# Kernel tuning notes

Measured on AMD Instinct MI355X. Metric: run time of the kernel, lower is better.

The kernel has to match this reference:

```python
import jax, jax.numpy as jnp
import numpy as np

B, S, T = 512, 1024, 64

def setup_inputs() -> dict:
    key = jax.random.key(0)
    k1, k2, k3 = jax.random.split(key, 3)
    emissions = jax.random.normal(k1, (B, S, T), dtype=jnp.float32)
    tags = jax.random.randint(k2, (B, S), 0, T, dtype=jnp.int32)
    mask = jnp.ones((B, S), dtype=jnp.float32)
    transitions = jax.random.normal(k3, (T, T), dtype=jnp.float32)
    return {"emissions": emissions, "tags": tags, "mask": mask, "transitions": transitions}

def _gold_score(emissions, tags, mask, transitions):
    # emit score of the gold tag at each position: (B, S)
    e = jnp.take_along_axis(emissions, tags[:, :, None], axis=2)[:, :, 0]
    # NOTE: original indexes transitions[curr, prev]
    trans = transitions[tags[:, 1:], tags[:, :-1]]  # (B, S-1)
    score = e[:, 0] * mask[:, 0]
    score = score + jnp.sum((trans + e[:, 1:]) * mask[:, 1:], axis=1)
    return score

def _partition(emissions, mask, transitions):
    # init: emissions at t=0, masked (matches original, which multiplies score by mask[:,0])
    score0 = emissions[:, 0] * mask[:, 0][:, None]  # (B, T)
    emis_rest = jnp.swapaxes(emissions[:, 1:], 0, 1)  # (S-1, B, T)
    mask_rest = jnp.swapaxes(mask[:, 1:], 0, 1)       # (S-1, B)

    def step(score, xs):
        emit, m = xs  # (B, T), (B,)
        # next[b, j] = logsumexp_i(score[b, i] + transitions[i, j])
        nxt = jax.nn.logsumexp(score[:, :, None] + transitions[None, :, :], axis=1)
        score = nxt + emit * m[:, None]
        return score, None

    score, _ = jax.lax.scan(step, score0, (emis_rest, mask_rest))
    return jax.nn.logsumexp(score, axis=1)  # (B,)

def reference(emissions, tags, mask, transitions):
    gold = _gold_score(emissions, tags, mask, transitions)
    fwd = _partition(emissions, mask, transitions)
    return jnp.mean(fwd - gold)
```

## Files before the change

kernel.cpp:

```cpp
#include <hip/hip_runtime.h>

#define BB 512
#define SS 1024
#define TT 64

__device__ __forceinline__ float wsum64(float v) {
#pragma unroll
  for (int off = 32; off > 0; off >>= 1) v += __shfl_xor(v, off, 64);
  return v;
}

#define E_LIST(M) \
  M(0) M(1) M(2) M(3) M(4) M(5) M(6) M(7) \
  M(8) M(9) M(10) M(11) M(12) M(13) M(14) M(15) \
  M(16) M(17) M(18) M(19) M(20) M(21) M(22) M(23) \
  M(24) M(25) M(26) M(27) M(28) M(29) M(30) M(31) \
  M(32) M(33) M(34) M(35) M(36) M(37) M(38) M(39) \
  M(40) M(41) M(42) M(43) M(44) M(45) M(46) M(47) \
  M(48) M(49) M(50) M(51) M(52) M(53) M(54) M(55) \
  M(56) M(57) M(58) M(59) M(60) M(61) M(62) M(63)

#define RL(i) __int_as_float(__builtin_amdgcn_readlane(pb_, (i)))

#define FMA4(i0, i1, i2, i3)          \
  a0 = fmaf(RL(i0), E##i0, a0);       \
  a1 = fmaf(RL(i1), E##i1, a1);       \
  a2 = fmaf(RL(i2), E##i2, a2);       \
  a3 = fmaf(RL(i3), E##i3, a3);

#define FMA_ALL                      \
  FMA4(0, 1, 2, 3)                   \
  FMA4(4, 5, 6, 7)                   \
  FMA4(8, 9, 10, 11)                 \
  FMA4(12, 13, 14, 15)               \
  FMA4(16, 17, 18, 19)               \
  FMA4(20, 21, 22, 23)               \
  FMA4(24, 25, 26, 27)               \
  FMA4(28, 29, 30, 31)               \
  FMA4(32, 33, 34, 35)               \
  FMA4(36, 37, 38, 39)               \
  FMA4(40, 41, 42, 43)               \
  FMA4(44, 45, 46, 47)               \
  FMA4(48, 49, 50, 51)               \
  FMA4(52, 53, 54, 55)               \
  FMA4(56, 57, 58, 59)               \
  FMA4(60, 61, 62, 63)

#define CRF_STEP(ev, mkv)                                                           \
  do {                                                                              \
    float f_ = __expf((ev) * (mkv));                                                \
    float pv_ = (DIR == 1) ? p * (f_ * inv) : p;                                    \
    int pb_ = __float_as_int(pv_);                                                  \
    float a0 = 0.f, a1 = 0.f, a2 = 0.f, a3 = 0.f;                                   \
    FMA_ALL                                                                         \
    float s_ = (a0 + a1) + (a2 + a3);                                               \
    p = (DIR == 0) ? s_ * (f_ * inv) : s_;                                          \
    float rn_ = __int_as_float(__builtin_amdgcn_readfirstlane(__float_as_int(s_))); \
    inv = __builtin_amdgcn_rcpf(rn_);                                               \
    float lg_ = __logf(rn_);                                                        \
    Lacc += lg_;                                                                    \
    lastlg = lg_;                                                                   \
  } while (0)

template <int DIR>
__device__ __forceinline__ void part_run(int b, int lane, const float* __restrict__ em,
                                         const float* __restrict__ mask,
                                         const float* __restrict__ trans,
                                         float* __restrict__ outv) {
  const float* tp = trans + (DIR == 0 ? lane : lane * TT);
#define EINIT(i) float E##i = __expf((DIR == 0) ? tp[(i)*TT] : tp[(i)]);
  E_LIST(EINIT)
#undef EINIT

  const float* emb = em + (size_t)b * SS * TT;
  const float* mkb = mask + (size_t)b * SS;

  constexpr int NST = (DIR == 0) ? (SS / 2 - 1) : (SS / 2);
  constexpr int S0 = (DIR == 0) ? 1 : (SS - 1);
  constexpr int SD = (DIR == 0) ? 1 : -1;
  constexpr int NG8 = NST / 8;
  constexpr int TAIL8 = NST & 7;

  float p = (DIR == 0) ? __expf(emb[lane] * mkb[0]) : 1.0f;
  float inv = 1.0f, Lacc = 0.0f, lastlg = 0.0f;

  float ebuf[8];
#pragma unroll
  for (int k = 0; k < 8; ++k) ebuf[k] = emb[(S0 + SD * k) * TT + lane];
  const float* ep = emb + (ptrdiff_t)(S0 + SD * 8) * TT + lane;

  float mv = 0.f;
  for (int t8 = 0; t8 < NG8; ++t8) {
    if ((t8 & 7) == 0) mv = mkb[S0 + SD * (t8 * 8 + lane)];
    int base = (t8 & 7) * 8;
#pragma unroll
    for (int k = 0; k < 8; ++k) {
      float e = ebuf[k];
      ebuf[k] = *ep;
      ep += SD * TT;
      float mk = __int_as_float(
          __builtin_amdgcn_readlane(__float_as_int(mv), base + k));
      CRF_STEP(e, mk);
    }
  }
  if constexpr (TAIL8 > 0) {
#pragma unroll
    for (int k = 0; k < TAIL8; ++k) {
      float e = ebuf[k];
      float mk = __int_as_float(
          __builtin_amdgcn_readlane(__float_as_int(mv), (NG8 & 7) * 8 + k));
      CRF_STEP(e, mk);
    }
  }

  outv[b * TT + lane] = __logf(p) + (Lacc - lastlg);
}

__global__ void __launch_bounds__(64, 1)
    fused_kernel(const float* __restrict__ em, const int* __restrict__ tags,
                 const float* __restrict__ mask, const float* __restrict__ trans,
                 float* __restrict__ alpha, float* __restrict__ beta,
                 float* __restrict__ gpart) {
  const int lane = threadIdx.x;
  const int bid = blockIdx.x;
  if (bid < 2 * BB) {
    const int b = bid >> 1;
    if ((bid & 1) == 0)
      part_run<0>(b, lane, em, mask, trans, alpha);
    else
      part_run<1>(b, lane, em, mask, trans, beta);
  } else {
    const int gid = bid - 2 * BB;
    const int b = gid >> 2, q = gid & 3;
    const int* tg = tags + b * SS;
    const float* mkb = mask + (size_t)b * SS;
    const float* emb = em + (size_t)b * SS * TT;
    float part = 0.f;
#pragma unroll
    for (int i = 0; i < 4; ++i) {
      int s = q * 256 + i * 64 + lane;
      int t1 = tg[s];
      float e = emb[s * TT + t1];
      float contrib = (s == 0) ? e : (trans[t1 * TT + tg[s - 1]] + e);
      part = fmaf(contrib, mkb[s], part);
    }
    part = wsum64(part);
    if (lane == 0) gpart[gid] = part;
  }
}

__global__ void combine_kernel(const float* __restrict__ alpha, const float* __restrict__ beta,
                               const float* __restrict__ gpart, float* __restrict__ out) {
  const int b = threadIdx.x;
  const float* av = alpha + b * TT;
  const float* bv = beta + b * TT;
  float m = -3.4e38f, s = 0.f;
#pragma unroll 8
  for (int j = 0; j < TT; ++j) {
    float v = av[j] + bv[j];
    float nm = fmaxf(m, v);
    s = s * __expf(m - nm) + __expf(v - nm);
    m = nm;
  }
  float Z = m + __logf(s);
  float g = gpart[4 * b] + gpart[4 * b + 1] + gpart[4 * b + 2] + gpart[4 * b + 3];
  float val = Z - g;
  val = wsum64(val);
  __shared__ float red[8];
  if ((threadIdx.x & 63) == 0) red[threadIdx.x >> 6] = val;
  __syncthreads();
  if (threadIdx.x == 0) {
    float t = 0.f;
#pragma unroll
    for (int w = 0; w < 8; ++w) t += red[w];
    out[0] = t * (1.0f / (float)BB);
  }
}

extern "C" void kernel_launch(void* const* d_in, const int* in_sizes, int n_in,
                              void* d_out, int out_size, void* d_ws, size_t ws_size,
                              hipStream_t stream) {
  const float* em = (const float*)d_in[0];
  const int* tags = (const int*)d_in[1];
  const float* mask = (const float*)d_in[2];
  const float* trans = (const float*)d_in[3];
  float* out = (float*)d_out;

  float* alpha = (float*)d_ws;
  float* beta = alpha + BB * TT;
  float* gpart = beta + BB * TT;

  fused_kernel<<<2 * BB + 4 * BB, TT, 0, stream>>>(em, tags, mask, trans, alpha, beta, gpart);
  combine_kernel<<<1, BB, 0, stream>>>(alpha, beta, gpart, out);
}
```

Before: 328.8 us.

## Broadcast recurrence state through LDS float4 reads instead of per-lane readlane

Each recurrence step now writes the 64-entry state vector to shared memory and reads it back as 16 broadcast float4 loads. This replaces 64 v_readlane scalar broadcasts per step, aiming to cut the scalar-broadcast cost and its associated hazards. The backward direction is restructured to apply the next position's emission factor before storing, which needs a one-step lookahead on emissions and mask. In exchange, an LDS write-then-read round trip now sits on the serial dependency chain of every step.

```diff
diff --git a/kernel.cpp b/kernel.cpp
--- a/kernel.cpp
+++ b/kernel.cpp
@@ -20,41 +20,48 @@
   M(48) M(49) M(50) M(51) M(52) M(53) M(54) M(55) \
   M(56) M(57) M(58) M(59) M(60) M(61) M(62) M(63)
 
-#define RL(i) __int_as_float(__builtin_amdgcn_readlane(pb_, (i)))
-
-#define FMA4(i0, i1, i2, i3)          \
-  a0 = fmaf(RL(i0), E##i0, a0);       \
-  a1 = fmaf(RL(i1), E##i1, a1);       \
-  a2 = fmaf(RL(i2), E##i2, a2);       \
-  a3 = fmaf(RL(i3), E##i3, a3);
-
-#define FMA_ALL                      \
-  FMA4(0, 1, 2, 3)                   \
-  FMA4(4, 5, 6, 7)                   \
-  FMA4(8, 9, 10, 11)                 \
-  FMA4(12, 13, 14, 15)               \
-  FMA4(16, 17, 18, 19)               \
-  FMA4(20, 21, 22, 23)               \
-  FMA4(24, 25, 26, 27)               \
-  FMA4(28, 29, 30, 31)               \
-  FMA4(32, 33, 34, 35)               \
-  FMA4(36, 37, 38, 39)               \
-  FMA4(40, 41, 42, 43)               \
-  FMA4(44, 45, 46, 47)               \
-  FMA4(48, 49, 50, 51)               \
-  FMA4(52, 53, 54, 55)               \
-  FMA4(56, 57, 58, 59)               \
-  FMA4(60, 61, 62, 63)
-
-#define CRF_STEP(ev, mkv)                                                           \
+#define RLF(v, i) __int_as_float(__builtin_amdgcn_readlane(__float_as_int(v), (i)))
+
+#define LOAD_ALLQ                                                     \
+  float4 q0 = pshv[0], q1 = pshv[1], q2 = pshv[2], q3 = pshv[3];      \
+  float4 q4 = pshv[4], q5 = pshv[5], q6 = pshv[6], q7 = pshv[7];      \
+  float4 q8 = pshv[8], q9 = pshv[9], q10 = pshv[10], q11 = pshv[11];  \
+  float4 q12 = pshv[12], q13 = pshv[13], q14 = pshv[14], q15 = pshv[15];
+
+#define FMAQ(qq, eA, eB, eC, eD) \
+  a0 = fmaf((qq).x, eA, a0);     \
+  a1 = fmaf((qq).y, eB, a1);     \
+  a2 = fmaf((qq).z, eC, a2);     \
+  a3 = fmaf((qq).w, eD, a3);
+
+#define FMA_ALLQ                     \
+  FMAQ(q0, E0, E1, E2, E3)           \
+  FMAQ(q1, E4, E5, E6, E7)           \
+  FMAQ(q2, E8, E9, E10, E11)         \
+  FMAQ(q3, E12, E13, E14, E15)       \
+  FMAQ(q4, E16, E17, E18, E19)       \
+  FMAQ(q5, E20, E21, E22, E23)       \
+  FMAQ(q6, E24, E25, E26, E27)       \
+  FMAQ(q7, E28, E29, E30, E31)       \
+  FMAQ(q8, E32, E33, E34, E35)       \
+  FMAQ(q9, E36, E37, E38, E39)       \
+  FMAQ(q10, E40, E41, E42, E43)      \
+  FMAQ(q11, E44, E45, E46, E47)      \
+  FMAQ(q12, E48, E49, E50, E51)      \
+  FMAQ(q13, E52, E53, E54, E55)      \
+  FMAQ(q14, E56, E57, E58, E59)      \
+  FMAQ(q15, E60, E61, E62, E63)
+
+#define CRF_STEP_FWD(ev, mkv)                                                       \
   do {                                                                              \
+    LOAD_ALLQ                                                                       \
     float f_ = __expf((ev) * (mkv));                                                \
-    float pv_ = (DIR == 1) ? p * (f_ * inv) : p;                                    \
-    int pb_ = __float_as_int(pv_);                                                  \
+    float fi_ = f_ * inv;                                                           \
     float a0 = 0.f, a1 = 0.f, a2 = 0.f, a3 = 0.f;                                   \
-    FMA_ALL                                                                         \
+    FMA_ALLQ                                                                        \
     float s_ = (a0 + a1) + (a2 + a3);                                               \
-    p = (DIR == 0) ? s_ * (f_ * inv) : s_;                                          \
+    p = s_ * fi_;                                                                   \
+    psh[lane] = p;                                                                  \
     float rn_ = __int_as_float(__builtin_amdgcn_readfirstlane(__float_as_int(s_))); \
     inv = __builtin_amdgcn_rcpf(rn_);                                               \
     float lg_ = __logf(rn_);                                                        \
@@ -62,11 +69,30 @@
     lastlg = lg_;                                                                   \
   } while (0)
 
+#define CRF_STEP_BWD(env, mknv)                                                     \
+  do {                                                                              \
+    LOAD_ALLQ                                                                       \
+    float fn_ = __expf((env) * (mknv));                                             \
+    float a0 = 0.f, a1 = 0.f, a2 = 0.f, a3 = 0.f;                                   \
+    FMA_ALLQ                                                                        \
+    float s_ = (a0 + a1) + (a2 + a3);                                               \
+    p = s_ * inv;                                                                   \
+    psh[lane] = p * fn_;                                                            \
+    float rn_ = __int_as_float(__builtin_amdgcn_readfirstlane(__float_as_int(s_))); \
+    inv = __builtin_amdgcn_rcpf(rn_);                                               \
+    float lg_ = __logf(rn_);                                                        \
+    Lacc += lg_;                                                                    \
+    lastlg = lg_;                                                                   \
+  } while (0)
+
 template <int DIR>
 __device__ __forceinline__ void part_run(int b, int lane, const float* __restrict__ em,
                                          const float* __restrict__ mask,
                                          const float* __restrict__ trans,
                                          float* __restrict__ outv) {
+  __shared__ float4 pshv[TT / 4];
+  float* psh = (float*)pshv;
+
   const float* tp = trans + (DIR == 0 ? lane : lane * TT);
 #define EINIT(i) float E##i = __expf((DIR == 0) ? tp[(i)*TT] : tp[(i)]);
   E_LIST(EINIT)
@@ -81,35 +107,55 @@
   constexpr int NG8 = NST / 8;
   constexpr int TAIL8 = NST & 7;
 
-  float p = (DIR == 0) ? __expf(emb[lane] * mkb[0]) : 1.0f;
-  float inv = 1.0f, Lacc = 0.0f, lastlg = 0.0f;
+  float p, inv = 1.0f, Lacc = 0.0f, lastlg = 0.0f;
 
   float ebuf[8];
 #pragma unroll
   for (int k = 0; k < 8; ++k) ebuf[k] = emb[(S0 + SD * k) * TT + lane];
   const float* ep = emb + (ptrdiff_t)(S0 + SD * 8) * TT + lane;
 
-  float mv = 0.f;
+  float mv = mkb[S0 + SD * lane];
+
+  if (DIR == 0) {
+    p = __expf(emb[lane] * mkb[0]);
+    psh[lane] = p;
+  } else {
+    p = 1.0f;
+    float mk1 = RLF(mv, 0);
+    float f1 = __expf(ebuf[0] * mk1);
+    psh[lane] = f1;
+  }
+
   for (int t8 = 0; t8 < NG8; ++t8) {
-    if ((t8 & 7) == 0) mv = mkb[S0 + SD * (t8 * 8 + lane)];
-    int base = (t8 & 7) * 8;
+    if (DIR == 0 && (t8 & 7) == 0) mv = mkb[S0 + SD * (t8 * 8 + lane)];
+    const int base = (t8 & 7) * 8;
 #pragma unroll
     for (int k = 0; k < 8; ++k) {
       float e = ebuf[k];
       ebuf[k] = *ep;
       ep += SD * TT;
-      float mk = __int_as_float(
-          __builtin_amdgcn_readlane(__float_as_int(mv), base + k));
-      CRF_STEP(e, mk);
+      if (DIR == 0) {
+        float mk = RLF(mv, base + k);
+        CRF_STEP_FWD(e, mk);
+      } else {
+        float mk_next;
+        if (base + k == 63) {
+          mv = mkb[S0 + SD * (t8 * 8 + 8 + lane)];
+          mk_next = RLF(mv, 0);
+        } else {
+          mk_next = RLF(mv, base + k + 1);
+        }
+        float e_next = ebuf[(k + 1) & 7];
+        CRF_STEP_BWD(e_next, mk_next);
+      }
     }
   }
   if constexpr (TAIL8 > 0) {
 #pragma unroll
     for (int k = 0; k < TAIL8; ++k) {
       float e = ebuf[k];
-      float mk = __int_as_float(
-          __builtin_amdgcn_readlane(__float_as_int(mv), (NG8 & 7) * 8 + k));
-      CRF_STEP(e, mk);
+      float mk = RLF(mv, (NG8 & 7) * 8 + k);
+      CRF_STEP_FWD(e, mk);
     }
   }
 
```

After: 376.5 us. 1.15x slower.

## Split each CRF recurrence step across two wavefronts with LDS exchange

Applied to the files above, without the earlier changes.

Each forward/backward chain now uses a 128-thread block where each wavefront holds half of the exp(transition) column (32 registers) and computes half of the 64-term dot product per step. The partial sums are exchanged through double-buffered shared memory with a __syncthreads every step. This halves the serial FMA/readlane chain per wave and lowers register pressure, but adds a block barrier and an LDS round trip on the critical path of every one of roughly 512 sequential steps. The gold-score blocks are adapted to 128 threads with a shared-memory reduction.

```diff
diff --git a/kernel.cpp b/kernel.cpp
--- a/kernel.cpp
+++ b/kernel.cpp
@@ -10,50 +10,41 @@
   return v;
 }
 
-#define E_LIST(M) \
+#define H_LIST(M) \
   M(0) M(1) M(2) M(3) M(4) M(5) M(6) M(7) \
   M(8) M(9) M(10) M(11) M(12) M(13) M(14) M(15) \
   M(16) M(17) M(18) M(19) M(20) M(21) M(22) M(23) \
-  M(24) M(25) M(26) M(27) M(28) M(29) M(30) M(31) \
-  M(32) M(33) M(34) M(35) M(36) M(37) M(38) M(39) \
-  M(40) M(41) M(42) M(43) M(44) M(45) M(46) M(47) \
-  M(48) M(49) M(50) M(51) M(52) M(53) M(54) M(55) \
-  M(56) M(57) M(58) M(59) M(60) M(61) M(62) M(63)
-
-#define RL(i) __int_as_float(__builtin_amdgcn_readlane(pb_, (i)))
-
-#define FMA4(i0, i1, i2, i3)          \
-  a0 = fmaf(RL(i0), E##i0, a0);       \
-  a1 = fmaf(RL(i1), E##i1, a1);       \
-  a2 = fmaf(RL(i2), E##i2, a2);       \
-  a3 = fmaf(RL(i3), E##i3, a3);
-
-#define FMA_ALL                      \
-  FMA4(0, 1, 2, 3)                   \
-  FMA4(4, 5, 6, 7)                   \
-  FMA4(8, 9, 10, 11)                 \
-  FMA4(12, 13, 14, 15)               \
-  FMA4(16, 17, 18, 19)               \
-  FMA4(20, 21, 22, 23)               \
-  FMA4(24, 25, 26, 27)               \
-  FMA4(28, 29, 30, 31)               \
-  FMA4(32, 33, 34, 35)               \
-  FMA4(36, 37, 38, 39)               \
-  FMA4(40, 41, 42, 43)               \
-  FMA4(44, 45, 46, 47)               \
-  FMA4(48, 49, 50, 51)               \
-  FMA4(52, 53, 54, 55)               \
-  FMA4(56, 57, 58, 59)               \
-  FMA4(60, 61, 62, 63)
-
-#define CRF_STEP(ev, mkv)                                                           \
+  M(24) M(25) M(26) M(27) M(28) M(29) M(30) M(31)
+
+#define RLW(i) __int_as_float(__builtin_amdgcn_readlane(pb_, (W) * 32 + (i)))
+
+#define FMAH4(i0, i1, i2, i3)    \
+  a0 = fmaf(RLW(i0), E##i0, a0); \
+  a1 = fmaf(RLW(i1), E##i1, a1); \
+  a2 = fmaf(RLW(i2), E##i2, a2); \
+  a3 = fmaf(RLW(i3), E##i3, a3);
+
+#define FMA_HALF        \
+  FMAH4(0, 1, 2, 3)     \
+  FMAH4(4, 5, 6, 7)     \
+  FMAH4(8, 9, 10, 11)   \
+  FMAH4(12, 13, 14, 15) \
+  FMAH4(16, 17, 18, 19) \
+  FMAH4(20, 21, 22, 23) \
+  FMAH4(24, 25, 26, 27) \
+  FMAH4(28, 29, 30, 31)
+
+#define CRF_STEP2(ev, mkv, BUF)                                                     \
   do {                                                                              \
     float f_ = __expf((ev) * (mkv));                                                \
     float pv_ = (DIR == 1) ? p * (f_ * inv) : p;                                    \
     int pb_ = __float_as_int(pv_);                                                  \
     float a0 = 0.f, a1 = 0.f, a2 = 0.f, a3 = 0.f;                                   \
-    FMA_ALL                                                                         \
-    float s_ = (a0 + a1) + (a2 + a3);                                               \
+    FMA_HALF                                                                        \
+    float h_ = (a0 + a1) + (a2 + a3);                                               \
+    xch[BUF][W][lane] = h_;                                                         \
+    __syncthreads();                                                                \
+    float s_ = h_ + xch[BUF][1 - W][lane];                                          \
     p = (DIR == 0) ? s_ * (f_ * inv) : s_;                                          \
     float rn_ = __int_as_float(__builtin_amdgcn_readfirstlane(__float_as_int(s_))); \
     inv = __builtin_amdgcn_rcpf(rn_);                                               \
@@ -62,14 +53,15 @@
     lastlg = lg_;                                                                   \
   } while (0)
 
-template <int DIR>
-__device__ __forceinline__ void part_run(int b, int lane, const float* __restrict__ em,
-                                         const float* __restrict__ mask,
-                                         const float* __restrict__ trans,
-                                         float* __restrict__ outv) {
+template <int DIR, int W>
+__device__ __forceinline__ void part_run2(int b, int lane, const float* __restrict__ em,
+                                          const float* __restrict__ mask,
+                                          const float* __restrict__ trans,
+                                          float* __restrict__ outv,
+                                          float (*xch)[2][TT]) {
   const float* tp = trans + (DIR == 0 ? lane : lane * TT);
-#define EINIT(i) float E##i = __expf((DIR == 0) ? tp[(i)*TT] : tp[(i)]);
-  E_LIST(EINIT)
+#define EINIT(i) float E##i = __expf((DIR == 0) ? tp[((W)*32 + (i)) * TT] : tp[(W)*32 + (i)]);
+  H_LIST(EINIT)
 #undef EINIT
 
   const float* emb = em + (size_t)b * SS * TT;
@@ -92,7 +84,7 @@
   float mv = 0.f;
   for (int t8 = 0; t8 < NG8; ++t8) {
     if ((t8 & 7) == 0) mv = mkb[S0 + SD * (t8 * 8 + lane)];
-    int base = (t8 & 7) * 8;
+    const int base = (t8 & 7) * 8;
 #pragma unroll
     for (int k = 0; k < 8; ++k) {
       float e = ebuf[k];
@@ -100,7 +92,11 @@
       ep += SD * TT;
       float mk = __int_as_float(
           __builtin_amdgcn_readlane(__float_as_int(mv), base + k));
-      CRF_STEP(e, mk);
+      if (k & 1) {
+        CRF_STEP2(e, mk, 1);
+      } else {
+        CRF_STEP2(e, mk, 0);
+      }
     }
   }
   if constexpr (TAIL8 > 0) {
@@ -109,26 +105,41 @@
       float e = ebuf[k];
       float mk = __int_as_float(
           __builtin_amdgcn_readlane(__float_as_int(mv), (NG8 & 7) * 8 + k));
-      CRF_STEP(e, mk);
-    }
-  }
-
-  outv[b * TT + lane] = __logf(p) + (Lacc - lastlg);
-}
-
-__global__ void __launch_bounds__(64, 1)
+      if (k & 1) {
+        CRF_STEP2(e, mk, 1);
+      } else {
+        CRF_STEP2(e, mk, 0);
+      }
+    }
+  }
+
+  if (W == 0) outv[b * TT + lane] = __logf(p) + (Lacc - lastlg);
+}
+
+__global__ void __launch_bounds__(128, 2)
     fused_kernel(const float* __restrict__ em, const int* __restrict__ tags,
                  const float* __restrict__ mask, const float* __restrict__ trans,
                  float* __restrict__ alpha, float* __restrict__ beta,
                  float* __restrict__ gpart) {
-  const int lane = threadIdx.x;
+  __shared__ float xch[2][2][TT];
+  __shared__ float gred[2];
+  const int tid = threadIdx.x;
   const int bid = blockIdx.x;
   if (bid < 2 * BB) {
     const int b = bid >> 1;
-    if ((bid & 1) == 0)
-      part_run<0>(b, lane, em, mask, trans, alpha);
-    else
-      part_run<1>(b, lane, em, mask, trans, beta);
+    const int lane = tid & 63;
+    const int w = tid >> 6;
+    if ((bid & 1) == 0) {
+      if (w == 0)
+        part_run2<0, 0>(b, lane, em, mask, trans, alpha, xch);
+      else
+        part_run2<0, 1>(b, lane, em, mask, trans, alpha, xch);
+    } else {
+      if (w == 0)
+        part_run2<1, 0>(b, lane, em, mask, trans, beta, xch);
+      else
+        part_run2<1, 1>(b, lane, em, mask, trans, beta, xch);
+    }
   } else {
     const int gid = bid - 2 * BB;
     const int b = gid >> 2, q = gid & 3;
@@ -137,15 +148,17 @@
     const float* emb = em + (size_t)b * SS * TT;
     float part = 0.f;
 #pragma unroll
-    for (int i = 0; i < 4; ++i) {
-      int s = q * 256 + i * 64 + lane;
+    for (int i = 0; i < 2; ++i) {
+      int s = q * 256 + i * 128 + tid;
       int t1 = tg[s];
       float e = emb[s * TT + t1];
       float contrib = (s == 0) ? e : (trans[t1 * TT + tg[s - 1]] + e);
       part = fmaf(contrib, mkb[s], part);
     }
     part = wsum64(part);
-    if (lane == 0) gpart[gid] = part;
+    if ((tid & 63) == 0) gred[tid >> 6] = part;
+    __syncthreads();
+    if (tid == 0) gpart[gid] = gred[0] + gred[1];
   }
 }
 
@@ -190,6 +203,6 @@
   float* beta = alpha + BB * TT;
   float* gpart = beta + BB * TT;
 
-  fused_kernel<<<2 * BB + 4 * BB, TT, 0, stream>>>(em, tags, mask, trans, alpha, beta, gpart);
+  fused_kernel<<<2 * BB + 4 * BB, 128, 0, stream>>>(em, tags, mask, trans, alpha, beta, gpart);
   combine_kernel<<<1, BB, 0, stream>>>(alpha, beta, gpart, out);
 }
```

Result: slower. 386.7 us (+17.6%).

## Process two batch sequences per wavefront to interleave independent recurrence chains

Applied to the files above, without the earlier changes.

Each partition wavefront now runs the forward or backward recurrence for two batch rows at once, interleaving their readlane and FMA chains. This halves the number of partition blocks from 1024 to 512 and gives the scheduler two independent dependency chains to hide readlane/FMA latency. The risk is reduced parallelism across CUs (512 waves on a 256-CU device) and higher register pressure from double state.

```diff
diff --git a/kernel.cpp b/kernel.cpp
--- a/kernel.cpp
+++ b/kernel.cpp
@@ -20,60 +20,102 @@
   M(48) M(49) M(50) M(51) M(52) M(53) M(54) M(55) \
   M(56) M(57) M(58) M(59) M(60) M(61) M(62) M(63)
 
-#define RL(i) __int_as_float(__builtin_amdgcn_readlane(pb_, (i)))
-
-#define FMA4(i0, i1, i2, i3)          \
-  a0 = fmaf(RL(i0), E##i0, a0);       \
-  a1 = fmaf(RL(i1), E##i1, a1);       \
-  a2 = fmaf(RL(i2), E##i2, a2);       \
-  a3 = fmaf(RL(i3), E##i3, a3);
-
-#define FMA_ALL                      \
-  FMA4(0, 1, 2, 3)                   \
-  FMA4(4, 5, 6, 7)                   \
-  FMA4(8, 9, 10, 11)                 \
-  FMA4(12, 13, 14, 15)               \
-  FMA4(16, 17, 18, 19)               \
-  FMA4(20, 21, 22, 23)               \
-  FMA4(24, 25, 26, 27)               \
-  FMA4(28, 29, 30, 31)               \
-  FMA4(32, 33, 34, 35)               \
-  FMA4(36, 37, 38, 39)               \
-  FMA4(40, 41, 42, 43)               \
-  FMA4(44, 45, 46, 47)               \
-  FMA4(48, 49, 50, 51)               \
-  FMA4(52, 53, 54, 55)               \
-  FMA4(56, 57, 58, 59)               \
-  FMA4(60, 61, 62, 63)
-
-#define CRF_STEP(ev, mkv)                                                           \
-  do {                                                                              \
-    float f_ = __expf((ev) * (mkv));                                                \
-    float pv_ = (DIR == 1) ? p * (f_ * inv) : p;                                    \
-    int pb_ = __float_as_int(pv_);                                                  \
-    float a0 = 0.f, a1 = 0.f, a2 = 0.f, a3 = 0.f;                                   \
-    FMA_ALL                                                                         \
-    float s_ = (a0 + a1) + (a2 + a3);                                               \
-    p = (DIR == 0) ? s_ * (f_ * inv) : s_;                                          \
-    float rn_ = __int_as_float(__builtin_amdgcn_readfirstlane(__float_as_int(s_))); \
-    inv = __builtin_amdgcn_rcpf(rn_);                                               \
-    float lg_ = __logf(rn_);                                                        \
-    Lacc += lg_;                                                                    \
-    lastlg = lg_;                                                                   \
+#define RLI(pb, i) __int_as_float(__builtin_amdgcn_readlane((pb), (i)))
+#define RLF(v, i) __int_as_float(__builtin_amdgcn_readlane(__float_as_int(v), (i)))
+
+#define GRP16(I0, I1, I2, I3, I4, I5, I6, I7, I8, I9, I10, I11, I12, I13, I14, I15) \
+  {                                                                                 \
+    float rA0 = RLI(pbA, I0), rA1 = RLI(pbA, I1), rA2 = RLI(pbA, I2),               \
+          rA3 = RLI(pbA, I3), rA4 = RLI(pbA, I4), rA5 = RLI(pbA, I5),               \
+          rA6 = RLI(pbA, I6), rA7 = RLI(pbA, I7), rA8 = RLI(pbA, I8),               \
+          rA9 = RLI(pbA, I9), rA10 = RLI(pbA, I10), rA11 = RLI(pbA, I11),           \
+          rA12 = RLI(pbA, I12), rA13 = RLI(pbA, I13), rA14 = RLI(pbA, I14),         \
+          rA15 = RLI(pbA, I15);                                                     \
+    float rB0 = RLI(pbB, I0), rB1 = RLI(pbB, I1), rB2 = RLI(pbB, I2),               \
+          rB3 = RLI(pbB, I3), rB4 = RLI(pbB, I4), rB5 = RLI(pbB, I5),               \
+          rB6 = RLI(pbB, I6), rB7 = RLI(pbB, I7), rB8 = RLI(pbB, I8),               \
+          rB9 = RLI(pbB, I9), rB10 = RLI(pbB, I10), rB11 = RLI(pbB, I11),           \
+          rB12 = RLI(pbB, I12), rB13 = RLI(pbB, I13), rB14 = RLI(pbB, I14),         \
+          rB15 = RLI(pbB, I15);                                                     \
+    aA0 = fmaf(rA0, E##I0, aA0);                                                    \
+    aA1 = fmaf(rA1, E##I1, aA1);                                                    \
+    aA2 = fmaf(rA2, E##I2, aA2);                                                    \
+    aA3 = fmaf(rA3, E##I3, aA3);                                                    \
+    aA0 = fmaf(rA4, E##I4, aA0);                                                    \
+    aA1 = fmaf(rA5, E##I5, aA1);                                                    \
+    aA2 = fmaf(rA6, E##I6, aA2);                                                    \
+    aA3 = fmaf(rA7, E##I7, aA3);                                                    \
+    aA0 = fmaf(rA8, E##I8, aA0);                                                    \
+    aA1 = fmaf(rA9, E##I9, aA1);                                                    \
+    aA2 = fmaf(rA10, E##I10, aA2);                                                  \
+    aA3 = fmaf(rA11, E##I11, aA3);                                                  \
+    aA0 = fmaf(rA12, E##I12, aA0);                                                  \
+    aA1 = fmaf(rA13, E##I13, aA1);                                                  \
+    aA2 = fmaf(rA14, E##I14, aA2);                                                  \
+    aA3 = fmaf(rA15, E##I15, aA3);                                                  \
+    aB0 = fmaf(rB0, E##I0, aB0);                                                    \
+    aB1 = fmaf(rB1, E##I1, aB1);                                                    \
+    aB2 = fmaf(rB2, E##I2, aB2);                                                    \
+    aB3 = fmaf(rB3, E##I3, aB3);                                                    \
+    aB0 = fmaf(rB4, E##I4, aB0);                                                    \
+    aB1 = fmaf(rB5, E##I5, aB1);                                                    \
+    aB2 = fmaf(rB6, E##I6, aB2);                                                    \
+    aB3 = fmaf(rB7, E##I7, aB3);                                                    \
+    aB0 = fmaf(rB8, E##I8, aB0);                                                    \
+    aB1 = fmaf(rB9, E##I9, aB1);                                                    \
+    aB2 = fmaf(rB10, E##I10, aB2);                                                  \
+    aB3 = fmaf(rB11, E##I11, aB3);                                                  \
+    aB0 = fmaf(rB12, E##I12, aB0);                                                  \
+    aB1 = fmaf(rB13, E##I13, aB1);                                                  \
+    aB2 = fmaf(rB14, E##I14, aB2);                                                  \
+    aB3 = fmaf(rB15, E##I15, aB3);                                                  \
+  }
+
+#define STEP_PAIR(eA, mkA, eB, mkB)                                                     \
+  do {                                                                                  \
+    float fA_ = __expf((eA) * (mkA));                                                   \
+    float fB_ = __expf((eB) * (mkB));                                                   \
+    float pvA_ = (DIR == 1) ? pA * (fA_ * invA) : pA;                                   \
+    float pvB_ = (DIR == 1) ? pB * (fB_ * invB) : pB;                                   \
+    int pbA = __float_as_int(pvA_);                                                     \
+    int pbB = __float_as_int(pvB_);                                                     \
+    float aA0 = 0.f, aA1 = 0.f, aA2 = 0.f, aA3 = 0.f;                                   \
+    float aB0 = 0.f, aB1 = 0.f, aB2 = 0.f, aB3 = 0.f;                                   \
+    GRP16(0, 1, 2, 3, 4, 5, 6, 7, 8, 9, 10, 11, 12, 13, 14, 15)                         \
+    GRP16(16, 17, 18, 19, 20, 21, 22, 23, 24, 25, 26, 27, 28, 29, 30, 31)               \
+    GRP16(32, 33, 34, 35, 36, 37, 38, 39, 40, 41, 42, 43, 44, 45, 46, 47)               \
+    GRP16(48, 49, 50, 51, 52, 53, 54, 55, 56, 57, 58, 59, 60, 61, 62, 63)               \
+    float sA_ = (aA0 + aA1) + (aA2 + aA3);                                              \
+    float sB_ = (aB0 + aB1) + (aB2 + aB3);                                              \
+    pA = (DIR == 0) ? sA_ * (fA_ * invA) : sA_;                                         \
+    pB = (DIR == 0) ? sB_ * (fB_ * invB) : sB_;                                         \
+    float rnA_ = __int_as_float(__builtin_amdgcn_readfirstlane(__float_as_int(sA_)));   \
+    float rnB_ = __int_as_float(__builtin_amdgcn_readfirstlane(__float_as_int(sB_)));   \
+    invA = __builtin_amdgcn_rcpf(rnA_);                                                 \
+    invB = __builtin_amdgcn_rcpf(rnB_);                                                 \
+    float lgA_ = __logf(rnA_);                                                          \
+    float lgB_ = __logf(rnB_);                                                          \
+    LaccA += lgA_;                                                                      \
+    LaccB += lgB_;                                                                      \
+    lastlgA = lgA_;                                                                     \
+    lastlgB = lgB_;                                                                     \
   } while (0)
 
 template <int DIR>
-__device__ __forceinline__ void part_run(int b, int lane, const float* __restrict__ em,
-                                         const float* __restrict__ mask,
-                                         const float* __restrict__ trans,
-                                         float* __restrict__ outv) {
+__device__ __forceinline__ void part_pair(int b0, int b1, int lane,
+                                          const float* __restrict__ em,
+                                          const float* __restrict__ mask,
+                                          const float* __restrict__ trans,
+                                          float* __restrict__ outv) {
   const float* tp = trans + (DIR == 0 ? lane : lane * TT);
 #define EINIT(i) float E##i = __expf((DIR == 0) ? tp[(i)*TT] : tp[(i)]);
   E_LIST(EINIT)
 #undef EINIT
 
-  const float* emb = em + (size_t)b * SS * TT;
-  const float* mkb = mask + (size_t)b * SS;
+  const float* embA = em + (size_t)b0 * SS * TT;
+  const float* embB = em + (size_t)b1 * SS * TT;
+  const float* mkbA = mask + (size_t)b0 * SS;
+  const float* mkbB = mask + (size_t)b1 * SS;
 
   constexpr int NST = (DIR == 0) ? (SS / 2 - 1) : (SS / 2);
   constexpr int S0 = (DIR == 0) ? 1 : (SS - 1);
@@ -81,39 +123,53 @@
   constexpr int NG8 = NST / 8;
   constexpr int TAIL8 = NST & 7;
 
-  float p = (DIR == 0) ? __expf(emb[lane] * mkb[0]) : 1.0f;
-  float inv = 1.0f, Lacc = 0.0f, lastlg = 0.0f;
-
-  float ebuf[8];
-#pragma unroll
-  for (int k = 0; k < 8; ++k) ebuf[k] = emb[(S0 + SD * k) * TT + lane];
-  const float* ep = emb + (ptrdiff_t)(S0 + SD * 8) * TT + lane;
-
-  float mv = 0.f;
+  float pA = (DIR == 0) ? __expf(embA[lane] * mkbA[0]) : 1.0f;
+  float pB = (DIR == 0) ? __expf(embB[lane] * mkbB[0]) : 1.0f;
+  float invA = 1.0f, invB = 1.0f;
+  float LaccA = 0.0f, LaccB = 0.0f, lastlgA = 0.0f, lastlgB = 0.0f;
+
+  float ebufA[8], ebufB[8];
+#pragma unroll
+  for (int k = 0; k < 8; ++k) {
+    ebufA[k] = embA[(S0 + SD * k) * TT + lane];
+    ebufB[k] = embB[(S0 + SD * k) * TT + lane];
+  }
+  const float* epA = embA + (ptrdiff_t)(S0 + SD * 8) * TT + lane;
+  const float* epB = embB + (ptrdiff_t)(S0 + SD * 8) * TT + lane;
+
+  float mvA = 0.f, mvB = 0.f;
   for (int t8 = 0; t8 < NG8; ++t8) {
-    if ((t8 & 7) == 0) mv = mkb[S0 + SD * (t8 * 8 + lane)];
-    int base = (t8 & 7) * 8;
+    if ((t8 & 7) == 0) {
+      mvA = mkbA[S0 + SD * (t8 * 8 + lane)];
+      mvB = mkbB[S0 + SD * (t8 * 8 + lane)];
+    }
+    const int base = (t8 & 7) * 8;
 #pragma unroll
     for (int k = 0; k < 8; ++k) {
-      float e = ebuf[k];
-      ebuf[k] = *ep;
-      ep += SD * TT;
-      float mk = __int_as_float(
-          __builtin_amdgcn_readlane(__float_as_int(mv), base + k));
-      CRF_STEP(e, mk);
+      float eA = ebufA[k];
+      float eB = ebufB[k];
+      ebufA[k] = *epA;
+      ebufB[k] = *epB;
+      epA += SD * TT;
+      epB += SD * TT;
+      float mkA = RLF(mvA, base + k);
+      float mkB = RLF(mvB, base + k);
+      STEP_PAIR(eA, mkA, eB, mkB);
     }
   }
   if constexpr (TAIL8 > 0) {
 #pragma unroll
     for (int k = 0; k < TAIL8; ++k) {
-      float e = ebuf[k];
-      float mk = __int_as_float(
-          __builtin_amdgcn_readlane(__float_as_int(mv), (NG8 & 7) * 8 + k));
-      CRF_STEP(e, mk);
-    }
-  }
-
-  outv[b * TT + lane] = __logf(p) + (Lacc - lastlg);
+      float eA = ebufA[k];
+      float eB = ebufB[k];
+      float mkA = RLF(mvA, (NG8 & 7) * 8 + k);
+      float mkB = RLF(mvB, (NG8 & 7) * 8 + k);
+      STEP_PAIR(eA, mkA, eB, mkB);
+    }
+  }
+
+  outv[b0 * TT + lane] = __logf(pA) + (LaccA - lastlgA);
+  outv[b1 * TT + lane] = __logf(pB) + (LaccB - lastlgB);
 }
 
 __global__ void __launch_bounds__(64, 1)
@@ -123,14 +179,15 @@
                  float* __restrict__ gpart) {
   const int lane = threadIdx.x;
   const int bid = blockIdx.x;
-  if (bid < 2 * BB) {
-    const int b = bid >> 1;
+  if (bid < BB) {
+    const int q = bid >> 1;
+    const int b0 = 2 * q, b1 = 2 * q + 1;
     if ((bid & 1) == 0)
-      part_run<0>(b, lane, em, mask, trans, alpha);
+      part_pair<0>(b0, b1, lane, em, mask, trans, alpha);
     else
-      part_run<1>(b, lane, em, mask, trans, beta);
+      part_pair<1>(b0, b1, lane, em, mask, trans, beta);
   } else {
-    const int gid = bid - 2 * BB;
+    const int gid = bid - BB;
     const int b = gid >> 2, q = gid & 3;
     const int* tg = tags + b * SS;
     const float* mkb = mask + (size_t)b * SS;
@@ -190,6 +247,6 @@
   float* beta = alpha + BB * TT;
   float* gpart = beta + BB * TT;
 
-  fused_kernel<<<2 * BB + 4 * BB, TT, 0, stream>>>(em, tags, mask, trans, alpha, beta, gpart);
+  fused_kernel<<<BB + 4 * BB, TT, 0, stream>>>(em, tags, mask, trans, alpha, beta, gpart);
   combine_kernel<<<1, BB, 0, stream>>>(alpha, beta, gpart, out);
 }
```

Result: slower. 479.2 us (+45.7%).
